# Kernel tuning notes

Hardware: AMD Instinct MI355X
Metric: run time of the kernel (lower is better)

## Reference

```python
import jax, jax.numpy as jnp
import numpy as np

DELTA = 2.5749
BN_EPS = 1e-5
N_LAYERS = 5


def _gin_pna_conv(x, src, dst, nW1, nb1, nW2, nb2, mW, mb):
    # x: [N, D]; src/dst: [E]
    N = x.shape[0]
    msgs = x[src]                                   # [E, D] gather (message = x_j)
    cnt = jax.ops.segment_sum(jnp.ones_like(dst, dtype=x.dtype), dst, num_segments=N)  # [N]
    c = jnp.maximum(cnt, 1.0)[:, None]              # guard isolated nodes
    sums = jax.ops.segment_sum(msgs, dst, num_segments=N)          # [N, D]
    maxs = jax.ops.segment_max(msgs, dst, num_segments=N)
    maxs = jnp.where(cnt[:, None] > 0, maxs, 0.0)   # empty segments -> 0 (torch_scatter behavior)
    means = sums / c
    sq_means = jax.ops.segment_sum(msgs * msgs, dst, num_segments=N) / c
    var = jax.nn.relu(sq_means - means * means)
    base = jnp.concatenate([sums, maxs, means, var], axis=1)        # [N, 4D]
    amp = (c / DELTA) * base                        # amplification scaler
    att = (DELTA / c) * base                        # attenuation scaler
    comb = jnp.concatenate([base, amp, att], axis=1)                # [N, 12D]
    agg = comb @ mW.T + mb                          # mlp: 12D -> D
    h = agg + x                                     # GIN: (1+eps)*x_r + aggr, eps=0
    h = jax.nn.relu(h @ nW1.T + nb1) @ nW2.T + nb2  # nn = Linear-ReLU-Linear
    return h


def _batchnorm(x, gamma, beta):
    mu = jnp.mean(x, axis=0)
    var = jnp.var(x, axis=0)
    return (x - mu) * jax.lax.rsqrt(var + BN_EPS) * gamma + beta


def setup_inputs() -> dict:
    key = jax.random.key(0)
    ks = jax.random.split(key, 12)
    N, E, D, G, OUT = 100000, 1600000, 64, 512, 16
    s = 0.05
    p = lambda k, shape: jax.random.normal(k, shape, dtype=jnp.float32) * s
    return {
        "x": jax.random.normal(ks[0], (N, D), dtype=jnp.float32),
        "edge_index": jax.random.randint(ks[1], (2, E), 0, N),
        "batch": jnp.sort(jax.random.randint(ks[2], (N,), 0, G)),
        "encW": p(ks[3], (D, D)), "encb": jnp.zeros((D,), jnp.float32),
        "nnW1": p(ks[4], (N_LAYERS, D, D)), "nnb1": jnp.zeros((N_LAYERS, D), jnp.float32),
        "nnW2": p(ks[5], (N_LAYERS, D, D)), "nnb2": jnp.zeros((N_LAYERS, D), jnp.float32),
        "mlpW": p(ks[6], (N_LAYERS, D, 12 * D)), "mlpb": jnp.zeros((N_LAYERS, D), jnp.float32),
        "bnG": jnp.ones((N_LAYERS, D), jnp.float32), "bnB": jnp.zeros((N_LAYERS, D), jnp.float32),
        "fc1W": p(ks[7], (D, D)), "fc1b": jnp.zeros((D,), jnp.float32),
        "fc2W": p(ks[8], (OUT, D)), "fc2b": jnp.zeros((OUT,), jnp.float32),
    }


def reference(x, edge_index, batch, encW, encb, nnW1, nnb1, nnW2, nnb2,
              mlpW, mlpb, bnG, bnB, fc1W, fc1b, fc2W, fc2b):
    NUM_GRAPHS = 512
    src, dst = edge_index[0], edge_index[1]
    h = x @ encW.T + encb                           # encoder
    for i in range(N_LAYERS):                       # fixed small layer loop
        h = jax.nn.relu(_gin_pna_conv(h, src, dst, nnW1[i], nnb1[i],
                                      nnW2[i], nnb2[i], mlpW[i], mlpb[i]))
        h = _batchnorm(h, bnG[i], bnB[i])
    g = jax.ops.segment_sum(h, batch, num_segments=NUM_GRAPHS)      # global_add_pool
    g = jax.nn.relu(g @ fc1W.T + fc1b)              # dropout is identity in eval mode
    return g @ fc2W.T + fc2b
```

## Files before the change

### kernel.cpp

```cpp
#include <hip/hip_runtime.h>
#include <hip/hip_bf16.h>
#include <hip/hip_fp16.h>

#define DELTA 2.5749f
#define BN_EPS 1e-5f

typedef __attribute__((ext_vector_type(8))) _Float16 f16x8;
typedef __attribute__((ext_vector_type(2))) _Float16 f16x2;
typedef __attribute__((ext_vector_type(4))) float f32x4;
typedef __attribute__((ext_vector_type(4))) int i32x4;

__device__ inline unsigned short f2h(float f) {
    union { _Float16 h; unsigned short u; } v;
    v.h = (_Float16)f;
    return v.u;
}

__global__ __launch_bounds__(256) void k_degree(const int* __restrict__ dst,
                                                int* __restrict__ deg, int E, int npp) {
    int part = blockIdx.x & 7;
    int lo = part * npp, hi = lo + npp;
    int stride = (gridDim.x >> 3) * 256 * 4;
    for (int e = ((blockIdx.x >> 3) * 256 + threadIdx.x) * 4; e < E; e += stride) {
        if (e + 3 < E) {
            i32x4 d4 = __builtin_nontemporal_load((const i32x4*)(dst + e));
            if (d4.x >= lo && d4.x < hi) atomicAdd(&deg[d4.x], 1);
            if (d4.y >= lo && d4.y < hi) atomicAdd(&deg[d4.y], 1);
            if (d4.z >= lo && d4.z < hi) atomicAdd(&deg[d4.z], 1);
            if (d4.w >= lo && d4.w < hi) atomicAdd(&deg[d4.w], 1);
        } else {
            for (int k = e; k < E; k++) {
                int d = __builtin_nontemporal_load(dst + k);
                if (d >= lo && d < hi) atomicAdd(&deg[d], 1);
            }
        }
    }
}

#define SCAN_B 1024
__global__ void k_scan_block(const int* __restrict__ deg, int* __restrict__ excl,
                             int* __restrict__ bsums, int total) {
    __shared__ int s[SCAN_B];
    int t = threadIdx.x, i = blockIdx.x * SCAN_B + t;
    int v = (i < total) ? deg[i] : 0;
    s[t] = v; __syncthreads();
    for (int off = 1; off < SCAN_B; off <<= 1) {
        int x = (t >= off) ? s[t - off] : 0;
        __syncthreads();
        s[t] += x;
        __syncthreads();
    }
    if (i < total) excl[i] = s[t] - v;
    if (t == SCAN_B - 1) bsums[blockIdx.x] = s[t];
}

__global__ void k_scan_tops(int* __restrict__ bsums, int nb) {
    __shared__ int s[SCAN_B];
    int t = threadIdx.x;
    int v = (t < nb) ? bsums[t] : 0;
    s[t] = v; __syncthreads();
    for (int off = 1; off < SCAN_B; off <<= 1) {
        int x = (t >= off) ? s[t - off] : 0;
        __syncthreads();
        s[t] += x;
        __syncthreads();
    }
    if (t < nb) bsums[t] = s[t] - v;
}

__global__ void k_scan_add(int* __restrict__ excl, const int* __restrict__ bsums,
                           int* __restrict__ cur, int total) {
    int i = blockIdx.x * SCAN_B + threadIdx.x;
    if (i < total) {
        int v = excl[i] + bsums[blockIdx.x];
        excl[i] = v;
        if (i < total - 1) cur[i] = v;
    }
}

__global__ __launch_bounds__(256) void k_fill(const int* __restrict__ src,
                                              const int* __restrict__ dst,
                                              int* __restrict__ cur,
                                              int* __restrict__ col, int E, int npp) {
    int part = blockIdx.x & 7;
    int lo = part * npp, hi = lo + npp;
    int stride = (gridDim.x >> 3) * 256 * 4;
    for (int e = ((blockIdx.x >> 3) * 256 + threadIdx.x) * 4; e < E; e += stride) {
        if (e + 3 < E) {
            i32x4 d4 = __builtin_nontemporal_load((const i32x4*)(dst + e));
            if (d4.x >= lo && d4.x < hi) {
                int p = atomicAdd(&cur[d4.x], 1);
                col[p] = __builtin_nontemporal_load(src + e);
            }
            if (d4.y >= lo && d4.y < hi) {
                int p = atomicAdd(&cur[d4.y], 1);
                col[p] = __builtin_nontemporal_load(src + e + 1);
            }
            if (d4.z >= lo && d4.z < hi) {
                int p = atomicAdd(&cur[d4.z], 1);
                col[p] = __builtin_nontemporal_load(src + e + 2);
            }
            if (d4.w >= lo && d4.w < hi) {
                int p = atomicAdd(&cur[d4.w], 1);
                col[p] = __builtin_nontemporal_load(src + e + 3);
            }
        } else {
            for (int k = e; k < E; k++) {
                int d = __builtin_nontemporal_load(dst + k);
                if (d >= lo && d < hi) {
                    int p = atomicAdd(&cur[d], 1);
                    col[p] = __builtin_nontemporal_load(src + k);
                }
            }
        }
    }
}

__global__ void k_castw(const float* __restrict__ w, unsigned short* __restrict__ o, int n4) {
    int i = blockIdx.x * 256 + threadIdx.x;
    if (i < n4) {
        float4 v = ((const float4*)w)[i];
        ushort4 r;
        r.x = f2h(v.x); r.y = f2h(v.y); r.z = f2h(v.z); r.w = f2h(v.w);
        ((ushort4*)o)[i] = r;
    }
}

#define ACC2(V)                                                            \
    do {                                                                   \
        mx = __builtin_elementwise_max(mx, V);                             \
        float x0 = (float)V[0], x1 = (float)V[1];                          \
        sa += x0; qa = fmaf(x0, x0, qa);                                   \
        sb += x1; qb = fmaf(x1, x1, qb);                                   \
    } while (0)

__global__ __launch_bounds__(256) void k_agg(const unsigned short* __restrict__ h16,
                                             const int* __restrict__ rowptr,
                                             const int* __restrict__ col,
                                             const float* __restrict__ bnstat,
                                             const float* __restrict__ gamma,
                                             const float* __restrict__ beta,
                                             float invN, int first,
                                             unsigned short* __restrict__ baseF,
                                             float* __restrict__ cnt, int N) {
    int t = threadIdx.x;
    int lane = t & 63;
    int half = lane >> 5;
    int fl = lane & 31;
    int node = blockIdx.x * 8 + (t >> 6) * 2 + half;
    if (node >= N) return;
    int fo2 = fl * 2;
    float scx, scy, shx, shy;
    if (first) {
        scx = 1.f; scy = 1.f; shx = 0.f; shy = 0.f;
    } else {
        float mu0 = bnstat[fo2] * invN, mu1 = bnstat[fo2 + 1] * invN;
        float v0 = bnstat[64 + fo2] * invN - mu0 * mu0;
        float v1 = bnstat[64 + fo2 + 1] * invN - mu1 * mu1;
        scx = rsqrtf(v0 + BN_EPS) * gamma[fo2];
        scy = rsqrtf(v1 + BN_EPS) * gamma[fo2 + 1];
        shx = beta[fo2] - mu0 * scx;
        shy = beta[fo2 + 1] - mu1 * scy;
    }
    const _Float16* hp = (const _Float16*)h16;
    int s0 = rowptr[node], s1 = rowptr[node + 1];
    int deg = s1 - s0;
    float sa = 0.f, sb = 0.f, qa = 0.f, qb = 0.f;
    f16x2 mx;
    mx[0] = (_Float16)(-65504.0f); mx[1] = (_Float16)(-65504.0f);
    const _Float16* hb = hp + fo2;
    int nfull = deg >> 3;

    f16x2 vA[8];
    int cN[8];
    if (nfull >= 1) {
        int cC[8];
        const int* cp = col + s0;
#pragma unroll
        for (int j = 0; j < 8; j++) cC[j] = cp[j];
        if (nfull >= 2) {
#pragma unroll
            for (int j = 0; j < 8; j++) cN[j] = cp[8 + j];
        }
#pragma unroll
        for (int j = 0; j < 8; j++) vA[j] = *(const f16x2*)(hb + ((size_t)(unsigned)cC[j] << 6));
    }
    for (int b = 1; b < nfull; b++) {
        int cNN[8];
        f16x2 vB[8];
        if (b + 1 < nfull) {
            const int* cp = col + s0 + (b + 1) * 8;
#pragma unroll
            for (int j = 0; j < 8; j++) cNN[j] = cp[j];
        }
#pragma unroll
        for (int j = 0; j < 8; j++) vB[j] = *(const f16x2*)(hb + ((size_t)(unsigned)cN[j] << 6));
#pragma unroll
        for (int j = 0; j < 8; j++) ACC2(vA[j]);
#pragma unroll
        for (int j = 0; j < 8; j++) { vA[j] = vB[j]; }
#pragma unroll
        for (int j = 0; j < 8; j++) { cN[j] = cNN[j]; }
    }
    if (nfull >= 1) {
#pragma unroll
        for (int j = 0; j < 8; j++) ACC2(vA[j]);
    }
    int tb = s0 + nfull * 8;
    int rem = s1 - tb;
    if (rem > 0) {
        int cT[8];
        f16x2 vT[8];
#pragma unroll
        for (int j = 0; j < 8; j++) {
            int idx = (tb + j < s1) ? (tb + j) : (s1 - 1);
            cT[j] = col[idx];
        }
#pragma unroll
        for (int j = 0; j < 8; j++) vT[j] = *(const f16x2*)(hb + ((size_t)(unsigned)cT[j] << 6));
#pragma unroll
        for (int j = 0; j < 8; j++) {
            if (j < rem) ACC2(vT[j]);
        }
    }

    float c = (float)(deg > 0 ? deg : 1);
    float ic = 1.f / c;
    float sum0, sum1, max0, max1, mean0, mean1, var0, var1;
    if (deg == 0) {
        sum0 = sum1 = max0 = max1 = mean0 = mean1 = var0 = var1 = 0.f;
    } else {
        sum0 = fmaf(scx, sa, c * shx);
        sum1 = fmaf(scy, sb, c * shy);
        max0 = fmaf(scx, (float)mx[0], shx);
        max1 = fmaf(scy, (float)mx[1], shy);
        float m0 = sa * ic, m1 = sb * ic;
        mean0 = fmaf(scx, m0, shx);
        mean1 = fmaf(scy, m1, shy);
        var0 = scx * scx * fmaxf(fmaf(-m0, m0, qa * ic), 0.f);
        var1 = scy * scy * fmaxf(fmaf(-m1, m1, qb * ic), 0.f);
    }
    size_t b = (size_t)node * 256 + fo2;
    ushort2 o;
    o.x = f2h(sum0); o.y = f2h(sum1);  *(ushort2*)(baseF + b) = o;
    o.x = f2h(max0); o.y = f2h(max1);  *(ushort2*)(baseF + b + 64) = o;
    o.x = f2h(mean0); o.y = f2h(mean1); *(ushort2*)(baseF + b + 128) = o;
    o.x = f2h(var0); o.y = f2h(var1);  *(ushort2*)(baseF + b + 192) = o;
    if (fl == 0) cnt[node] = c;
}

__global__ __launch_bounds__(256) void k_mlp(const unsigned short* __restrict__ baseF,
                                             const float* __restrict__ cnt,
                                             const unsigned short* __restrict__ mWF,
                                             const float* __restrict__ mb,
                                             const unsigned short* __restrict__ hres16,
                                             const float* __restrict__ bnstatPrev,
                                             const float* __restrict__ gammaP,
                                             const float* __restrict__ betaP,
                                             float invN, int first,
                                             const unsigned short* __restrict__ w1F,
                                             const float* __restrict__ b1,
                                             const unsigned short* __restrict__ w2F,
                                             const float* __restrict__ b2,
                                             float* __restrict__ bnstat,
                                             unsigned short* __restrict__ hOut16, int N) {
    __shared__ char smem[49152];
    _Float16* ldsW = (_Float16*)smem;
    _Float16* bufA = (_Float16*)(smem + 12288);
    _Float16* bufB = bufA + 128 * 72;
    float* red = (float*)smem;

    int t = threadIdx.x;
    int wave = t >> 6, lane = t & 63;
    int r16 = lane & 15, quad = lane >> 4;
    int n0 = blockIdx.x * 128;
    int m0 = n0 + wave * 32;

    const _Float16* aptr0 = (const _Float16*)baseF + (size_t)(m0 + r16) * 256 + quad * 8;
    const _Float16* aptr1 = aptr0 + 16 * 256;
    f32x4 acc0[12], acc1[12];
#pragma unroll
    for (int i = 0; i < 12; i++) {
        acc0[i] = (f32x4){0.f, 0.f, 0.f, 0.f};
        acc1[i] = (f32x4){0.f, 0.f, 0.f, 0.f};
    }
    f16x8 aC0 = *(const f16x8*)(aptr0);
    f16x8 aC1 = *(const f16x8*)(aptr1);

#pragma unroll 1
    for (int sc = 0; sc < 8; sc++) {
        if (sc) __syncthreads();
#pragma unroll
        for (int j = 0; j < 3; j++) {
            int rec = wave * 3 + j;
            int mat = rec >> 2, nt = rec & 3;
            uint4 v = *(const uint4*)(mWF + (size_t)(nt * 16 + r16) * 768 + mat * 256
                                      + sc * 32 + quad * 8);
            *(uint4*)((unsigned short*)ldsW + rec * 512 + lane * 8) = v;
        }
        __syncthreads();
        f16x8 aN0, aN1;
        if (sc < 7) {
            aN0 = *(const f16x8*)(aptr0 + (sc + 1) * 32);
            aN1 = *(const f16x8*)(aptr1 + (sc + 1) * 32);
        }
#pragma unroll
        for (int tile = 0; tile < 12; tile++) {
            f16x8 wF = *(const f16x8*)(ldsW + tile * 512 + lane * 8);
            acc0[tile] = __builtin_amdgcn_mfma_f32_16x16x32_f16(aC0, wF, acc0[tile], 0, 0, 0);
            acc1[tile] = __builtin_amdgcn_mfma_f32_16x16x32_f16(aC1, wF, acc1[tile], 0, 0, 0);
        }
        aC0 = aN0; aC1 = aN1;
    }
    __syncthreads();

    {
        int nl = t >> 1, fo = (t & 1) * 32;
        int gn = n0 + nl;
        uint4* dp = (uint4*)(bufA + nl * 72 + fo);
        if (gn < N) {
            const uint4* sp = (const uint4*)(hres16 + (size_t)gn * 64 + fo);
            dp[0] = sp[0]; dp[1] = sp[1]; dp[2] = sp[2]; dp[3] = sp[3];
        } else {
            uint4 z = make_uint4(0, 0, 0, 0);
            dp[0] = z; dp[1] = z; dp[2] = z; dp[3] = z;
        }
    }
    __syncthreads();

    float scf[4], shf[4], mbv[4];
#pragma unroll
    for (int nt = 0; nt < 4; nt++) {
        int f = nt * 16 + r16;
        mbv[nt] = mb[f];
        if (first) {
            scf[nt] = 1.f; shf[nt] = 0.f;
        } else {
            float mu = bnstatPrev[f] * invN;
            float var = bnstatPrev[64 + f] * invN - mu * mu;
            float s = rsqrtf(var + BN_EPS) * gammaP[f];
            scf[nt] = s; shf[nt] = betaP[f] - mu * s;
        }
    }
#pragma unroll
    for (int mt = 0; mt < 2; mt++) {
#pragma unroll
        for (int i = 0; i < 4; i++) {
            int nl = wave * 32 + mt * 16 + quad * 4 + i;
            int gn = n0 + nl;
            if (gn < N) {
                float c = cnt[gn];
                float amp = c / DELTA, att = DELTA / c;
                f32x4* a = mt ? acc1 : acc0;
#pragma unroll
                for (int nt = 0; nt < 4; nt++) {
                    int f = nt * 16 + r16;
                    float r = (float)bufA[nl * 72 + f];
                    float v = a[nt][i] + amp * a[4 + nt][i] + att * a[8 + nt][i]
                            + mbv[nt] + fmaf(r, scf[nt], shf[nt]);
                    bufA[nl * 72 + f] = (_Float16)v;
                }
            }
        }
    }
    __syncthreads();

    f32x4 accN[8];
#pragma unroll
    for (int i = 0; i < 8; i++) accN[i] = (f32x4){0.f, 0.f, 0.f, 0.f};
#pragma unroll
    for (int s = 0; s < 2; s++) {
        f16x8 fA0 = *(const f16x8*)(bufA + (wave * 32 + r16) * 72 + s * 32 + quad * 8);
        f16x8 fA1 = *(const f16x8*)(bufA + (wave * 32 + 16 + r16) * 72 + s * 32 + quad * 8);
#pragma unroll
        for (int nt = 0; nt < 4; nt++) {
            f16x8 wB = *(const f16x8*)((const _Float16*)w1F + (size_t)(nt * 16 + r16) * 64
                                       + s * 32 + quad * 8);
            accN[nt]     = __builtin_amdgcn_mfma_f32_16x16x32_f16(fA0, wB, accN[nt], 0, 0, 0);
            accN[4 + nt] = __builtin_amdgcn_mfma_f32_16x16x32_f16(fA1, wB, accN[4 + nt], 0, 0, 0);
        }
    }
    float b1v[4];
#pragma unroll
    for (int nt = 0; nt < 4; nt++) b1v[nt] = b1[nt * 16 + r16];
#pragma unroll
    for (int mt = 0; mt < 2; mt++) {
#pragma unroll
        for (int i = 0; i < 4; i++) {
            int nl = wave * 32 + mt * 16 + quad * 4 + i;
#pragma unroll
            for (int nt = 0; nt < 4; nt++) {
                float v = fmaxf(accN[mt * 4 + nt][i] + b1v[nt], 0.f);
                bufB[nl * 72 + nt * 16 + r16] = (_Float16)v;
            }
        }
    }
    __syncthreads();

    f32x4 accM[8];
#pragma unroll
    for (int i = 0; i < 8; i++) accM[i] = (f32x4){0.f, 0.f, 0.f, 0.f};
#pragma unroll
    for (int s = 0; s < 2; s++) {
        f16x8 fA0 = *(const f16x8*)(bufB + (wave * 32 + r16) * 72 + s * 32 + quad * 8);
        f16x8 fA1 = *(const f16x8*)(bufB + (wave * 32 + 16 + r16) * 72 + s * 32 + quad * 8);
#pragma unroll
        for (int nt = 0; nt < 4; nt++) {
            f16x8 wB = *(const f16x8*)((const _Float16*)w2F + (size_t)(nt * 16 + r16) * 64
                                       + s * 32 + quad * 8);
            accM[nt]     = __builtin_amdgcn_mfma_f32_16x16x32_f16(fA0, wB, accM[nt], 0, 0, 0);
            accM[4 + nt] = __builtin_amdgcn_mfma_f32_16x16x32_f16(fA1, wB, accM[4 + nt], 0, 0, 0);
        }
    }
    float b2v[4], s1[4], s2[4];
#pragma unroll
    for (int nt = 0; nt < 4; nt++) {
        b2v[nt] = b2[nt * 16 + r16]; s1[nt] = 0.f; s2[nt] = 0.f;
    }
#pragma unroll
    for (int mt = 0; mt < 2; mt++) {
#pragma unroll
        for (int i = 0; i < 4; i++) {
            int nl = wave * 32 + mt * 16 + quad * 4 + i;
            bool ok = (n0 + nl) < N;
#pragma unroll
            for (int nt = 0; nt < 4; nt++) {
                float v = fmaxf(accM[mt * 4 + nt][i] + b2v[nt], 0.f);
                if (ok) { s1[nt] += v; s2[nt] = fmaf(v, v, s2[nt]); }
                bufA[nl * 72 + nt * 16 + r16] = (_Float16)v;
            }
        }
    }
#pragma unroll
    for (int nt = 0; nt < 4; nt++) {
        int row = wave * 4 + quad;
        red[row * 64 + nt * 16 + r16] = s1[nt];
        red[1024 + row * 64 + nt * 16 + r16] = s2[nt];
    }
    __syncthreads();

    {
        int nl = t >> 1, fo = (t & 1) * 32;
        int gn = n0 + nl;
        if (gn < N) {
            const uint4* sp = (const uint4*)(bufA + nl * 72 + fo);
            uint4* dp = (uint4*)(hOut16 + (size_t)gn * 64 + fo);
            dp[0] = sp[0]; dp[1] = sp[1]; dp[2] = sp[2]; dp[3] = sp[3];
        }
    }
    if (t < 128) {
        int d = t & 63, part = t >> 6;
        float tot = 0.f;
#pragma unroll
        for (int r = 0; r < 16; r++) tot += red[part * 1024 + r * 64 + d];
        atomicAdd(&bnstat[part * 64 + d], tot);
    }
}

#define FMA16(ACC0, ACC1, ACC2, ACC3, A, W)                                \
    do {                                                                   \
        ACC0.x = fmaf(A.x, W.x, ACC0.x); ACC0.y = fmaf(A.x, W.y, ACC0.y);  \
        ACC0.z = fmaf(A.x, W.z, ACC0.z); ACC0.w = fmaf(A.x, W.w, ACC0.w);  \
        ACC1.x = fmaf(A.y, W.x, ACC1.x); ACC1.y = fmaf(A.y, W.y, ACC1.y);  \
        ACC1.z = fmaf(A.y, W.z, ACC1.z); ACC1.w = fmaf(A.y, W.w, ACC1.w);  \
        ACC2.x = fmaf(A.z, W.x, ACC2.x); ACC2.y = fmaf(A.z, W.y, ACC2.y);  \
        ACC2.z = fmaf(A.z, W.z, ACC2.z); ACC2.w = fmaf(A.z, W.w, ACC2.w);  \
        ACC3.x = fmaf(A.w, W.x, ACC3.x); ACC3.y = fmaf(A.w, W.y, ACC3.y);  \
        ACC3.z = fmaf(A.w, W.z, ACC3.z); ACC3.w = fmaf(A.w, W.w, ACC3.w);  \
    } while (0)

__global__ __launch_bounds__(256) void k_gemm64(const float* __restrict__ in,
                                                const float* __restrict__ W,
                                                const float* __restrict__ bias,
                                                unsigned short* __restrict__ out16, int N) {
    __shared__ float sInT[64][64];
    __shared__ float sWT[64][64];
    int t = threadIdx.x;
    int tx = t & 15, ty = t >> 4;
    int n0 = blockIdx.x * 64;
    int c4 = tx * 4;
#pragma unroll
    for (int ch = 0; ch < 4; ch++) {
        int row = ch * 16 + ty;
        float4 v = make_float4(0.f, 0.f, 0.f, 0.f);
        if (n0 + row < N) v = *(const float4*)(in + (size_t)(n0 + row) * 64 + c4);
        sInT[c4 + 0][row] = v.x; sInT[c4 + 1][row] = v.y;
        sInT[c4 + 2][row] = v.z; sInT[c4 + 3][row] = v.w;
        float4 w = *(const float4*)(W + (size_t)row * 64 + c4);
        sWT[c4 + 0][row] = w.x; sWT[c4 + 1][row] = w.y;
        sWT[c4 + 2][row] = w.z; sWT[c4 + 3][row] = w.w;
    }
    __syncthreads();
    float4 acc0 = make_float4(0.f, 0.f, 0.f, 0.f);
    float4 acc1 = acc0, acc2 = acc0, acc3 = acc0;
#pragma unroll 8
    for (int k = 0; k < 64; k++) {
        float4 a = *(const float4*)(&sInT[k][ty * 4]);
        float4 w = *(const float4*)(&sWT[k][tx * 4]);
        FMA16(acc0, acc1, acc2, acc3, a, w);
    }
    float4 b4 = *(const float4*)(bias + tx * 4);
#pragma unroll
    for (int i = 0; i < 4; i++) {
        int n = n0 + ty * 4 + i;
        if (n < N) {
            float4 v = (i == 0) ? acc0 : (i == 1) ? acc1 : (i == 2) ? acc2 : acc3;
            v.x += b4.x; v.y += b4.y; v.z += b4.z; v.w += b4.w;
            ushort4 o;
            o.x = f2h(v.x); o.y = f2h(v.y); o.z = f2h(v.z); o.w = f2h(v.w);
            *(ushort4*)(out16 + (size_t)n * 64 + tx * 4) = o;
        }
    }
}

__global__ void k_pool(const unsigned short* __restrict__ h16, const int* __restrict__ batch,
                       const float* __restrict__ bnstat, const float* __restrict__ gamma,
                       const float* __restrict__ beta, float invN,
                       float* __restrict__ g, int N) {
    int d = threadIdx.x & 63, r = threadIdx.x >> 6;
    float mu = bnstat[d] * invN;
    float var = bnstat[64 + d] * invN - mu * mu;
    float sc = rsqrtf(var + BN_EPS) * gamma[d];
    float sh = beta[d] - mu * sc;
    const _Float16* hp = (const _Float16*)h16;
    int nbase = blockIdx.x * 32;
    float acc = 0.f;
    int gcur = -1;
    for (int i = 0; i < 8; i++) {
        int n = nbase + i * 4 + r;
        if (n < N) {
            int gb = batch[n];
            if (gb != gcur) {
                if (gcur >= 0) atomicAdd(&g[gcur * 64 + d], acc);
                acc = 0.f; gcur = gb;
            }
            acc += fmaf((float)hp[(size_t)n * 64 + d], sc, sh);
        }
    }
    if (gcur >= 0) atomicAdd(&g[gcur * 64 + d], acc);
}

__global__ void k_head(const float* __restrict__ g, const float* __restrict__ fc1W,
                       const float* __restrict__ fc1b, const float* __restrict__ fc2W,
                       const float* __restrict__ fc2b, float* __restrict__ out) {
    __shared__ float sg[64], sg1[64];
    int gi = blockIdx.x, t = threadIdx.x;
    sg[t] = g[gi * 64 + t];
    __syncthreads();
    float a = fc1b[t];
    for (int k = 0; k < 64; k++) a = fmaf(sg[k], fc1W[t * 64 + k], a);
    sg1[t] = fmaxf(a, 0.f);
    __syncthreads();
    if (t < 16) {
        float o = fc2b[t];
        for (int k = 0; k < 64; k++) o = fmaf(sg1[k], fc2W[t * 64 + k], o);
        out[gi * 16 + t] = o;
    }
}

extern "C" void kernel_launch(void* const* d_in, const int* in_sizes, int n_in,
                              void* d_out, int out_size, void* d_ws, size_t ws_size,
                              hipStream_t stream) {
    const float* x       = (const float*)d_in[0];
    const int*   eidx    = (const int*)d_in[1];
    const int*   batch   = (const int*)d_in[2];
    const float* encW    = (const float*)d_in[3];
    const float* encb    = (const float*)d_in[4];
    const float* nnW1    = (const float*)d_in[5];
    const float* nnb1    = (const float*)d_in[6];
    const float* nnW2    = (const float*)d_in[7];
    const float* nnb2    = (const float*)d_in[8];
    const float* mlpW    = (const float*)d_in[9];
    const float* mlpb    = (const float*)d_in[10];
    const float* bnG     = (const float*)d_in[11];
    const float* bnB     = (const float*)d_in[12];
    const float* fc1W    = (const float*)d_in[13];
    const float* fc1b    = (const float*)d_in[14];
    const float* fc2W    = (const float*)d_in[15];
    const float* fc2b    = (const float*)d_in[16];
    float* out = (float*)d_out;

    const int N = in_sizes[0] / 64;
    const int E = in_sizes[1] / 2;
    const int G = 512;
    const int* src = eidx;
    const int* dst = eidx + E;
    const int npp = (N + 7) / 8;
    const float invN = 1.f / (float)N;

    char* ws = (char*)d_ws;
    size_t off = 0;
    auto alloc = [&](size_t bytes) { size_t r = off; off = (off + bytes + 255) & ~(size_t)255; return r; };
    int*   deg     = (int*)(ws + alloc((size_t)(N + 1) * 4));
    int*   rowptr  = (int*)(ws + alloc((size_t)(N + 1) * 4));
    int*   bsums   = (int*)(ws + alloc(1024 * 4));
    int*   fill    = (int*)(ws + alloc((size_t)N * 4));
    int*   col     = (int*)(ws + alloc((size_t)E * 4));
    float* cnt     = (float*)(ws + alloc((size_t)N * 4));
    unsigned short* baseF = (unsigned short*)(ws + alloc((size_t)N * 256 * 2 + 131072));
    unsigned short* hC16 = (unsigned short*)(ws + alloc((size_t)N * 64 * 2 + 32768));
    unsigned short* mWF  = (unsigned short*)(ws + alloc((size_t)5 * 64 * 768 * 2));
    unsigned short* nW1F = (unsigned short*)(ws + alloc((size_t)5 * 64 * 64 * 2));
    unsigned short* nW2F = (unsigned short*)(ws + alloc((size_t)5 * 64 * 64 * 2));
    float* bnstats = (float*)(ws + alloc(5 * 128 * 4));
    float* gpool   = (float*)(ws + alloc((size_t)G * 64 * 4));

    hipMemsetAsync(deg, 0, (size_t)(N + 1) * 4, stream);
    hipMemsetAsync(bnstats, 0, 5 * 128 * 4, stream);
    hipMemsetAsync(gpool, 0, (size_t)G * 64 * 4, stream);

    int total = N + 1;
    int nscan = (total + SCAN_B - 1) / SCAN_B;
    int ngrid64 = (N + 63) / 64;
    int ngrid128 = (N + 127) / 128;

    k_degree<<<2048, 256, 0, stream>>>(dst, deg, E, npp);
    k_scan_block<<<nscan, SCAN_B, 0, stream>>>(deg, rowptr, bsums, total);
    k_scan_tops<<<1, SCAN_B, 0, stream>>>(bsums, nscan);
    k_scan_add<<<nscan, SCAN_B, 0, stream>>>(rowptr, bsums, fill, total);
    k_fill<<<2048, 256, 0, stream>>>(src, dst, fill, col, E, npp);

    k_castw<<<240, 256, 0, stream>>>(mlpW, mWF, 61440);
    k_castw<<<20, 256, 0, stream>>>(nnW1, nW1F, 5120);
    k_castw<<<20, 256, 0, stream>>>(nnW2, nW2F, 5120);

    k_gemm64<<<ngrid64, 256, 0, stream>>>(x, encW, encb, hC16, N);

    for (int i = 0; i < 5; i++) {
        const float* bsPrev = (i == 0) ? bnstats : bnstats + (i - 1) * 128;
        const float* gP = (i == 0) ? bnG : bnG + (i - 1) * 64;
        const float* bP = (i == 0) ? bnB : bnB + (i - 1) * 64;
        int first = (i == 0) ? 1 : 0;
        k_agg<<<(N + 7) / 8, 256, 0, stream>>>(hC16, rowptr, col, bsPrev, gP, bP,
                                               invN, first, baseF, cnt, N);
        k_mlp<<<ngrid128, 256, 0, stream>>>(baseF, cnt,
                                            mWF + (size_t)i * 64 * 768, mlpb + i * 64,
                                            hC16, bsPrev, gP, bP, invN, first,
                                            nW1F + (size_t)i * 4096, nnb1 + i * 64,
                                            nW2F + (size_t)i * 4096, nnb2 + i * 64,
                                            bnstats + i * 128, hC16, N);
    }

    k_pool<<<(N + 31) / 32, 256, 0, stream>>>(hC16, batch, bnstats + 4 * 128,
                                              bnG + 4 * 64, bnB + 4 * 64, invN, gpool, N);
    k_head<<<G, 64, 0, stream>>>(gpool, fc1W, fc1b, fc2W, fc2b, out);
}
```

Measured before the change: 760.5 us.

## Pre-bin edges by destination partition before degree count and CSR fill

Adds a binning pass that scatters each edge's (dst, src) into one of eight per-partition buckets using shared-memory histograms. Degree counting and CSR fill then read only their own partition's bucket instead of each rereading the whole edge list eight times with a range filter. This cuts redundant global reads of dst/src but costs an extra pass that writes 2E ints. The bucket capacity is fixed with a margin (E/8 + E/64 + 256), which holds for uniform random destinations but could overflow on skewed inputs.

```diff
diff --git a/kernel.cpp b/kernel.cpp
--- a/kernel.cpp
+++ b/kernel.cpp
@@ -8,7 +8,6 @@
 typedef __attribute__((ext_vector_type(8))) _Float16 f16x8;
 typedef __attribute__((ext_vector_type(2))) _Float16 f16x2;
 typedef __attribute__((ext_vector_type(4))) float f32x4;
-typedef __attribute__((ext_vector_type(4))) int i32x4;
 
 __device__ inline unsigned short f2h(float f) {
     union { _Float16 h; unsigned short u; } v;
@@ -16,24 +15,58 @@
     return v.u;
 }
 
-__global__ __launch_bounds__(256) void k_degree(const int* __restrict__ dst,
-                                                int* __restrict__ deg, int E, int npp) {
+__global__ __launch_bounds__(256) void k_bin(const int* __restrict__ dst,
+                                             const int* __restrict__ src,
+                                             int* __restrict__ bDst,
+                                             int* __restrict__ bSrc,
+                                             int* __restrict__ bcnt,
+                                             int E, int npp, int cap, int CS) {
+    __shared__ int hist[8], cur[8];
+    int t = threadIdx.x;
+    if (t < 8) hist[t] = 0;
+    __syncthreads();
+    int s0 = blockIdx.x * CS, s1 = min(s0 + CS, E);
+    for (int e = s0 + t; e < s1; e += 256) {
+        int p = dst[e] / npp;
+        atomicAdd(&hist[p], 1);
+    }
+    __syncthreads();
+    if (t < 8) cur[t] = atomicAdd(&bcnt[t], hist[t]);
+    __syncthreads();
+    for (int e = s0 + t; e < s1; e += 256) {
+        int d = dst[e];
+        int p = d / npp;
+        int pos = atomicAdd(&cur[p], 1);
+        bDst[p * cap + pos] = d;
+        bSrc[p * cap + pos] = src[e];
+    }
+}
+
+__global__ __launch_bounds__(256) void k_degree_b(const int* __restrict__ bDst,
+                                                  const int* __restrict__ bcnt,
+                                                  int* __restrict__ deg, int cap) {
     int part = blockIdx.x & 7;
-    int lo = part * npp, hi = lo + npp;
-    int stride = (gridDim.x >> 3) * 256 * 4;
-    for (int e = ((blockIdx.x >> 3) * 256 + threadIdx.x) * 4; e < E; e += stride) {
-        if (e + 3 < E) {
-            i32x4 d4 = __builtin_nontemporal_load((const i32x4*)(dst + e));
-            if (d4.x >= lo && d4.x < hi) atomicAdd(&deg[d4.x], 1);
-            if (d4.y >= lo && d4.y < hi) atomicAdd(&deg[d4.y], 1);
-            if (d4.z >= lo && d4.z < hi) atomicAdd(&deg[d4.z], 1);
-            if (d4.w >= lo && d4.w < hi) atomicAdd(&deg[d4.w], 1);
-        } else {
-            for (int k = e; k < E; k++) {
-                int d = __builtin_nontemporal_load(dst + k);
-                if (d >= lo && d < hi) atomicAdd(&deg[d], 1);
-            }
-        }
+    int n = bcnt[part];
+    const int* bp = bDst + part * cap;
+    int stride = (gridDim.x >> 3) * 256;
+    for (int i = (blockIdx.x >> 3) * 256 + threadIdx.x; i < n; i += stride)
+        atomicAdd(&deg[bp[i]], 1);
+}
+
+__global__ __launch_bounds__(256) void k_fill_b(const int* __restrict__ bDst,
+                                                const int* __restrict__ bSrc,
+                                                const int* __restrict__ bcnt,
+                                                int* __restrict__ cur,
+                                                int* __restrict__ col, int cap) {
+    int part = blockIdx.x & 7;
+    int n = bcnt[part];
+    const int* bd = bDst + part * cap;
+    const int* bs = bSrc + part * cap;
+    int stride = (gridDim.x >> 3) * 256;
+    for (int i = (blockIdx.x >> 3) * 256 + threadIdx.x; i < n; i += stride) {
+        int d = bd[i];
+        int pos = atomicAdd(&cur[d], 1);
+        col[pos] = bs[i];
     }
 }
 
@@ -75,44 +108,6 @@
         int v = excl[i] + bsums[blockIdx.x];
         excl[i] = v;
         if (i < total - 1) cur[i] = v;
-    }
-}
-
-__global__ __launch_bounds__(256) void k_fill(const int* __restrict__ src,
-                                              const int* __restrict__ dst,
-                                              int* __restrict__ cur,
-                                              int* __restrict__ col, int E, int npp) {
-    int part = blockIdx.x & 7;
-    int lo = part * npp, hi = lo + npp;
-    int stride = (gridDim.x >> 3) * 256 * 4;
-    for (int e = ((blockIdx.x >> 3) * 256 + threadIdx.x) * 4; e < E; e += stride) {
-        if (e + 3 < E) {
-            i32x4 d4 = __builtin_nontemporal_load((const i32x4*)(dst + e));
-            if (d4.x >= lo && d4.x < hi) {
-                int p = atomicAdd(&cur[d4.x], 1);
-                col[p] = __builtin_nontemporal_load(src + e);
-            }
-            if (d4.y >= lo && d4.y < hi) {
-                int p = atomicAdd(&cur[d4.y], 1);
-                col[p] = __builtin_nontemporal_load(src + e + 1);
-            }
-            if (d4.z >= lo && d4.z < hi) {
-                int p = atomicAdd(&cur[d4.z], 1);
-                col[p] = __builtin_nontemporal_load(src + e + 2);
-            }
-            if (d4.w >= lo && d4.w < hi) {
-                int p = atomicAdd(&cur[d4.w], 1);
-                col[p] = __builtin_nontemporal_load(src + e + 3);
-            }
-        } else {
-            for (int k = e; k < E; k++) {
-                int d = __builtin_nontemporal_load(dst + k);
-                if (d >= lo && d < hi) {
-                    int p = atomicAdd(&cur[d], 1);
-                    col[p] = __builtin_nontemporal_load(src + k);
-                }
-            }
-        }
     }
 }
 
@@ -587,6 +582,7 @@
     const int* dst = eidx + E;
     const int npp = (N + 7) / 8;
     const float invN = 1.f / (float)N;
+    const int cap = E / 8 + E / 64 + 256;
 
     char* ws = (char*)d_ws;
     size_t off = 0;
@@ -596,6 +592,9 @@
     int*   bsums   = (int*)(ws + alloc(1024 * 4));
     int*   fill    = (int*)(ws + alloc((size_t)N * 4));
     int*   col     = (int*)(ws + alloc((size_t)E * 4));
+    int*   bDst    = (int*)(ws + alloc((size_t)cap * 8 * 4));
+    int*   bSrc    = (int*)(ws + alloc((size_t)cap * 8 * 4));
+    int*   bcnt    = (int*)(ws + alloc(8 * 4));
     float* cnt     = (float*)(ws + alloc((size_t)N * 4));
     unsigned short* baseF = (unsigned short*)(ws + alloc((size_t)N * 256 * 2 + 131072));
     unsigned short* hC16 = (unsigned short*)(ws + alloc((size_t)N * 64 * 2 + 32768));
@@ -606,6 +605,7 @@
     float* gpool   = (float*)(ws + alloc((size_t)G * 64 * 4));
 
     hipMemsetAsync(deg, 0, (size_t)(N + 1) * 4, stream);
+    hipMemsetAsync(bcnt, 0, 8 * 4, stream);
     hipMemsetAsync(bnstats, 0, 5 * 128 * 4, stream);
     hipMemsetAsync(gpool, 0, (size_t)G * 64 * 4, stream);
 
@@ -613,12 +613,14 @@
     int nscan = (total + SCAN_B - 1) / SCAN_B;
     int ngrid64 = (N + 63) / 64;
     int ngrid128 = (N + 127) / 128;
-
-    k_degree<<<2048, 256, 0, stream>>>(dst, deg, E, npp);
+    int CS = (E + 2047) / 2048;
+
+    k_bin<<<2048, 256, 0, stream>>>(dst, src, bDst, bSrc, bcnt, E, npp, cap, CS);
+    k_degree_b<<<2048, 256, 0, stream>>>(bDst, bcnt, deg, cap);
     k_scan_block<<<nscan, SCAN_B, 0, stream>>>(deg, rowptr, bsums, total);
     k_scan_tops<<<1, SCAN_B, 0, stream>>>(bsums, nscan);
     k_scan_add<<<nscan, SCAN_B, 0, stream>>>(rowptr, bsums, fill, total);
-    k_fill<<<2048, 256, 0, stream>>>(src, dst, fill, col, E, npp);
+    k_fill_b<<<2048, 256, 0, stream>>>(bDst, bSrc, bcnt, fill, col, cap);
 
     k_castw<<<240, 256, 0, stream>>>(mlpW, mWF, 61440);
     k_castw<<<20, 256, 0, stream>>>(nnW1, nW1F, 5120);
```

After: 784.5 us. +3.1%, slower.
